# Kernel optimization log

Hardware: AMD Instinct MI355X
Metric: run time of the kernel (lower is better)

The kernel has to match this reference:

```python
import jax, jax.numpy as jnp
import numpy as np

BASE_P = 0.99
MIN_P = 0.9


def setup_inputs() -> dict:
    key = jax.random.key(0)
    k1, k2, k3 = jax.random.split(key, 3)
    B, T, C = 32, 4096, 256
    return {
        "student_latents": jax.random.normal(k1, (B, T, C), dtype=jnp.float32),
        "teacher_latents": jax.random.normal(k2, (B, T, C), dtype=jnp.float32),
        "risk_coef": jax.random.uniform(k3, (B,), dtype=jnp.float32),
    }


def reference(student_latents, teacher_latents, risk_coef):
    # 1) Epistemic uncertainty: per-token MSE between student and teacher  [B, T]
    delta = jnp.mean((student_latents - teacher_latents) ** 2, axis=-1)
    uncertainty = jnp.clip(delta * 2.0, 0.0, 1.0)
    # 2) Distrust = max(U, risk * U)  [B, T]
    distrust = jnp.maximum(uncertainty, risk_coef[:, None] * uncertainty)
    # 3) Dynamic percentile per sample  [B]
    distrust_b = jnp.mean(distrust, axis=1)
    p_eff = BASE_P - (BASE_P - MIN_P) * distrust_b
    # 4) Per-sample quantile threshold of |x| over flattened (T*C), then clamp.
    B = student_latents.shape[0]
    s = jnp.abs(student_latents).reshape(B, -1).astype(jnp.float32)
    # torch detaches before quantile -> no gradient through the threshold
    thresh = jax.lax.stop_gradient(
        jax.vmap(lambda a, q: jnp.quantile(a, q))(s, p_eff.astype(jnp.float32))
    )  # [B], linear interpolation matches torch.quantile default
    t = thresh[:, None, None].astype(student_latents.dtype)
    return jnp.clip(student_latents, -t, t)
```

## Files before the change

kernel.cpp:

```cpp
#include <hip/hip_runtime.h>
#include <stdint.h>

#define B_ 32
#define T_ 4096
#define C_ 256
#define N_ (T_*C_)
#define NB 8192

#define HIST_BYTES (B_*NB*4)
#define USUM_OFF   (HIST_BYTES)
#define THR_OFF    (USUM_OFF + 128)

__global__ __launch_bounds__(512, 6) void k1_uncert_hist(
    const float* __restrict__ s, const float* __restrict__ t,
    float* __restrict__ usum, unsigned* __restrict__ ghist)
{
    __shared__ unsigned lh[NB];
    __shared__ float wu[8];
    const int tid = threadIdx.x;
    #pragma unroll
    for (int k = tid; k < NB; k += 512) lh[k] = 0;
    __syncthreads();

    const int b = blockIdx.x >> 5;
    const size_t base4 = (size_t)blockIdx.x * 8192;
    const float4* s4 = (const float4*)s + base4;
    const float4* t4 = (const float4*)t + base4;
    const int lane = tid & 63, wid = tid >> 6;

    float uacc = 0.f;
    #pragma unroll 2
    for (int it = 0; it < 8; ++it) {
        const int i0 = it*1024 + wid*128 + lane;
        float4 a0 = s4[i0];
        float4 a1 = s4[i0 + 64];
        float4 c0 = t4[i0];
        float4 c1 = t4[i0 + 64];

        float d0 = a0.x-c0.x, d1 = a0.y-c0.y, d2 = a0.z-c0.z, d3 = a0.w-c0.w;
        float sum0 = d0*d0 + d1*d1 + d2*d2 + d3*d3;
        float e0 = a1.x-c1.x, e1 = a1.y-c1.y, e2 = a1.z-c1.z, e3 = a1.w-c1.w;
        float sum1 = e0*e0 + e1*e1 + e2*e2 + e3*e3;

        atomicAdd(&lh[(__float_as_uint(a0.x) & 0x7fffffffu) >> 18], 1u);
        atomicAdd(&lh[(__float_as_uint(a0.y) & 0x7fffffffu) >> 18], 1u);
        atomicAdd(&lh[(__float_as_uint(a0.z) & 0x7fffffffu) >> 18], 1u);
        atomicAdd(&lh[(__float_as_uint(a0.w) & 0x7fffffffu) >> 18], 1u);
        atomicAdd(&lh[(__float_as_uint(a1.x) & 0x7fffffffu) >> 18], 1u);
        atomicAdd(&lh[(__float_as_uint(a1.y) & 0x7fffffffu) >> 18], 1u);
        atomicAdd(&lh[(__float_as_uint(a1.z) & 0x7fffffffu) >> 18], 1u);
        atomicAdd(&lh[(__float_as_uint(a1.w) & 0x7fffffffu) >> 18], 1u);

        #pragma unroll
        for (int m = 1; m < 64; m <<= 1) {
            sum0 += __shfl_xor(sum0, m, 64);
            sum1 += __shfl_xor(sum1, m, 64);
        }
        if (lane == 0)
            uacc += fminf(sum0 * (1.0f/128.0f), 1.0f)
                  + fminf(sum1 * (1.0f/128.0f), 1.0f);
    }
    if (lane == 0) wu[wid] = uacc;
    __syncthreads();
    if (tid == 0) {
        float a = 0.f;
        #pragma unroll
        for (int w = 0; w < 8; ++w) a += wu[w];
        atomicAdd(&usum[b], a);
    }
    unsigned* gh = ghist + (size_t)b * NB;
    #pragma unroll
    for (int k = tid; k < NB; k += 512) {
        unsigned c = lh[k];
        if (c) atomicAdd(&gh[k], c);
    }
}

__global__ __launch_bounds__(256) void k2_thresh(
    const unsigned* __restrict__ ghist, const float* __restrict__ usum,
    const float* __restrict__ risk, float* __restrict__ thr)
{
    __shared__ unsigned lh[NB];
    __shared__ unsigned part[256];
    __shared__ unsigned pref[257];
    const int b = blockIdx.x, tid = threadIdx.x;
    const unsigned* gh = ghist + (size_t)b * NB;
    for (int j = tid; j < NB; j += 256) lh[j] = gh[j];
    __syncthreads();
    unsigned sl = 0;
    #pragma unroll
    for (int k = 0; k < 32; ++k) sl += lh[tid*32 + k];
    part[tid] = sl;
    __syncthreads();
    if (tid == 0) {
        unsigned acc = 0;
        for (int i = 0; i < 256; ++i) { pref[i] = acc; acc += part[i]; }
        pref[256] = acc;

        float distrust = usum[b] * fmaxf(1.f, risk[b]) * (1.0f/(float)T_);
        double p = 0.99 - 0.09 * (double)distrust;
        double pos = p * (double)(N_ - 1);
        unsigned i0 = (unsigned)pos;
        float g = (float)(pos - (double)i0);

        auto orderstat = [&](unsigned rk) -> float {
            int seg = 0;
            while (seg < 255 && pref[seg+1] <= rk) ++seg;
            unsigned cum = pref[seg];
            int bin = seg*32 + 31;
            unsigned cnt = 1;
            #pragma unroll
            for (int k = 0; k < 32; ++k) {
                unsigned c = lh[seg*32 + k];
                if (cum + c > rk) { bin = seg*32 + k; cnt = c; break; }
                cum += c;
            }
            float lo = __uint_as_float((unsigned)bin << 18);
            float hi = __uint_as_float((unsigned)(bin + 1) << 18);
            unsigned j = rk - cum;
            return lo + ((float)(j + 1) / (float)(cnt + 1)) * (hi - lo);
        };
        float v0 = orderstat(i0);
        float v1 = orderstat(i0 + 1);
        thr[b] = v0 + g * (v1 - v0);
    }
}

__global__ __launch_bounds__(256) void k3_clip(
    const float* __restrict__ s, const float* __restrict__ thr,
    float* __restrict__ out)
{
    const size_t idx4 = (size_t)blockIdx.x * 256 + threadIdx.x;
    const int b = (int)(idx4 >> 18);
    const float t = thr[b];
    float4 a = ((const float4*)s)[idx4];
    a.x = fminf(fmaxf(a.x, -t), t);
    a.y = fminf(fmaxf(a.y, -t), t);
    a.z = fminf(fmaxf(a.z, -t), t);
    a.w = fminf(fmaxf(a.w, -t), t);
    ((float4*)out)[idx4] = a;
}

extern "C" void kernel_launch(void* const* d_in, const int* in_sizes, int n_in,
                              void* d_out, int out_size, void* d_ws, size_t ws_size,
                              hipStream_t stream) {
    const float* s    = (const float*)d_in[0];
    const float* t    = (const float*)d_in[1];
    const float* risk = (const float*)d_in[2];
    float* out = (float*)d_out;
    char* ws = (char*)d_ws;

    unsigned* hist = (unsigned*)(ws);
    float*    usum = (float*)(ws + USUM_OFF);
    float*    thr  = (float*)(ws + THR_OFF);

    hipMemsetAsync(ws, 0, HIST_BYTES + 256, stream);

    k1_uncert_hist<<<B_*32, 512, 0, stream>>>(s, t, usum, hist);
    k2_thresh<<<B_, 256, 0, stream>>>(hist, usum, risk, thr);
    k3_clip<<<B_*N_/4/256, 256, 0, stream>>>(s, thr, out);
}
```

Baseline: 367.8 us.

## Pack histogram counters, prefetch loads, parallelize threshold scan, widen clip kernel

```diff
diff --git a/kernel.cpp b/kernel.cpp
--- a/kernel.cpp
+++ b/kernel.cpp
@@ -11,56 +11,82 @@
 #define USUM_OFF   (HIST_BYTES)
 #define THR_OFF    (USUM_OFF + 128)
 
-__global__ __launch_bounds__(512, 6) void k1_uncert_hist(
+typedef float f32x4 __attribute__((ext_vector_type(4)));
+
+__global__ __launch_bounds__(512, 8) void k1_uncert_hist(
     const float* __restrict__ s, const float* __restrict__ t,
     float* __restrict__ usum, unsigned* __restrict__ ghist)
 {
-    __shared__ unsigned lh[NB];
+    __shared__ unsigned lhist[4096];
+    __shared__ float part[64*65];
     __shared__ float wu[8];
     const int tid = threadIdx.x;
     #pragma unroll
-    for (int k = tid; k < NB; k += 512) lh[k] = 0;
-    __syncthreads();
-
-    const int b = blockIdx.x >> 5;
-    const size_t base4 = (size_t)blockIdx.x * 8192;
-    const float4* s4 = (const float4*)s + base4;
-    const float4* t4 = (const float4*)t + base4;
+    for (int k = tid; k < 4096; k += 512) lhist[k] = 0;
+    __syncthreads();
+
+    const int b = blockIdx.x >> 6;
+    const size_t base4 = (size_t)blockIdx.x * 4096;
+    const f32x4* s4 = (const f32x4*)s + base4;
+    const f32x4* t4 = (const f32x4*)t + base4;
     const int lane = tid & 63, wid = tid >> 6;
 
-    float uacc = 0.f;
-    #pragma unroll 2
-    for (int it = 0; it < 8; ++it) {
-        const int i0 = it*1024 + wid*128 + lane;
-        float4 a0 = s4[i0];
-        float4 a1 = s4[i0 + 64];
-        float4 c0 = t4[i0];
-        float4 c1 = t4[i0 + 64];
-
-        float d0 = a0.x-c0.x, d1 = a0.y-c0.y, d2 = a0.z-c0.z, d3 = a0.w-c0.w;
-        float sum0 = d0*d0 + d1*d1 + d2*d2 + d3*d3;
-        float e0 = a1.x-c1.x, e1 = a1.y-c1.y, e2 = a1.z-c1.z, e3 = a1.w-c1.w;
-        float sum1 = e0*e0 + e1*e1 + e2*e2 + e3*e3;
-
-        atomicAdd(&lh[(__float_as_uint(a0.x) & 0x7fffffffu) >> 18], 1u);
-        atomicAdd(&lh[(__float_as_uint(a0.y) & 0x7fffffffu) >> 18], 1u);
-        atomicAdd(&lh[(__float_as_uint(a0.z) & 0x7fffffffu) >> 18], 1u);
-        atomicAdd(&lh[(__float_as_uint(a0.w) & 0x7fffffffu) >> 18], 1u);
-        atomicAdd(&lh[(__float_as_uint(a1.x) & 0x7fffffffu) >> 18], 1u);
-        atomicAdd(&lh[(__float_as_uint(a1.y) & 0x7fffffffu) >> 18], 1u);
-        atomicAdd(&lh[(__float_as_uint(a1.z) & 0x7fffffffu) >> 18], 1u);
-        atomicAdd(&lh[(__float_as_uint(a1.w) & 0x7fffffffu) >> 18], 1u);
-
-        #pragma unroll
-        for (int m = 1; m < 64; m <<= 1) {
-            sum0 += __shfl_xor(sum0, m, 64);
-            sum1 += __shfl_xor(sum1, m, 64);
-        }
-        if (lane == 0)
-            uacc += fminf(sum0 * (1.0f/128.0f), 1.0f)
-                  + fminf(sum1 * (1.0f/128.0f), 1.0f);
-    }
-    if (lane == 0) wu[wid] = uacc;
+    int i = wid*128 + lane;
+    f32x4 a0 = s4[i];
+    f32x4 a1 = s4[i + 64];
+    f32x4 c0 = __builtin_nontemporal_load(t4 + i);
+    f32x4 c1 = __builtin_nontemporal_load(t4 + i + 64);
+
+    #pragma unroll
+    for (int it = 0; it < 4; ++it) {
+        f32x4 b0, b1, d0, d1;
+        const int inext = i + 1024;
+        if (it < 3) {
+            b0 = s4[inext];
+            b1 = s4[inext + 64];
+            d0 = __builtin_nontemporal_load(t4 + inext);
+            d1 = __builtin_nontemporal_load(t4 + inext + 64);
+        }
+
+        float dx = a0.x-c0.x, dy = a0.y-c0.y, dz = a0.z-c0.z, dw = a0.w-c0.w;
+        float sum0 = dx*dx + dy*dy + dz*dz + dw*dw;
+        float ex = a1.x-c1.x, ey = a1.y-c1.y, ez = a1.z-c1.z, ew = a1.w-c1.w;
+        float sum1 = ex*ex + ey*ey + ez*ez + ew*ew;
+
+        {
+            unsigned u;
+            u = __float_as_uint(a0.x); atomicAdd(&lhist[(u>>19)&0xFFF], 1u << (((u>>18)&1u)<<4));
+            u = __float_as_uint(a0.y); atomicAdd(&lhist[(u>>19)&0xFFF], 1u << (((u>>18)&1u)<<4));
+            u = __float_as_uint(a0.z); atomicAdd(&lhist[(u>>19)&0xFFF], 1u << (((u>>18)&1u)<<4));
+            u = __float_as_uint(a0.w); atomicAdd(&lhist[(u>>19)&0xFFF], 1u << (((u>>18)&1u)<<4));
+            u = __float_as_uint(a1.x); atomicAdd(&lhist[(u>>19)&0xFFF], 1u << (((u>>18)&1u)<<4));
+            u = __float_as_uint(a1.y); atomicAdd(&lhist[(u>>19)&0xFFF], 1u << (((u>>18)&1u)<<4));
+            u = __float_as_uint(a1.z); atomicAdd(&lhist[(u>>19)&0xFFF], 1u << (((u>>18)&1u)<<4));
+            u = __float_as_uint(a1.w); atomicAdd(&lhist[(u>>19)&0xFFF], 1u << (((u>>18)&1u)<<4));
+        }
+
+        const int tk = it*16 + wid*2;
+        part[tk*65 + lane]     = sum0;
+        part[(tk+1)*65 + lane] = sum1;
+
+        if (it < 3) { a0 = b0; a1 = b1; c0 = d0; c1 = d1; }
+        i = inext;
+    }
+    __syncthreads();
+
+    {
+        const int tok = tid >> 3, q = tid & 7;
+        const float* pp = &part[tok*65 + q*8];
+        float ps = pp[0]+pp[1]+pp[2]+pp[3]+pp[4]+pp[5]+pp[6]+pp[7];
+        ps += __shfl_xor(ps, 1, 64);
+        ps += __shfl_xor(ps, 2, 64);
+        ps += __shfl_xor(ps, 4, 64);
+        float u = fminf(ps * (1.0f/128.0f), 1.0f);
+        u += __shfl_xor(u, 8, 64);
+        u += __shfl_xor(u, 16, 64);
+        u += __shfl_xor(u, 32, 64);
+        if (lane == 0) wu[wid] = u;
+    }
     __syncthreads();
     if (tid == 0) {
         float a = 0.f;
@@ -68,11 +94,16 @@
         for (int w = 0; w < 8; ++w) a += wu[w];
         atomicAdd(&usum[b], a);
     }
+
     unsigned* gh = ghist + (size_t)b * NB;
     #pragma unroll
-    for (int k = tid; k < NB; k += 512) {
-        unsigned c = lh[k];
-        if (c) atomicAdd(&gh[k], c);
+    for (int w = tid; w < 4096; w += 512) {
+        const unsigned pc = lhist[w];
+        if (pc) {
+            const unsigned lo = pc & 0xFFFFu, hi = pc >> 16;
+            if (lo) atomicAdd(&gh[2*w],   lo);
+            if (hi) atomicAdd(&gh[2*w+1], hi);
+        }
     }
 }
 
@@ -81,64 +112,79 @@
     const float* __restrict__ risk, float* __restrict__ thr)
 {
     __shared__ unsigned lh[NB];
-    __shared__ unsigned part[256];
-    __shared__ unsigned pref[257];
+    __shared__ unsigned sc[256];
+    __shared__ float res[2];
     const int b = blockIdx.x, tid = threadIdx.x;
     const unsigned* gh = ghist + (size_t)b * NB;
     for (int j = tid; j < NB; j += 256) lh[j] = gh[j];
     __syncthreads();
-    unsigned sl = 0;
-    #pragma unroll
-    for (int k = 0; k < 32; ++k) sl += lh[tid*32 + k];
-    part[tid] = sl;
-    __syncthreads();
-    if (tid == 0) {
-        unsigned acc = 0;
-        for (int i = 0; i < 256; ++i) { pref[i] = acc; acc += part[i]; }
-        pref[256] = acc;
-
-        float distrust = usum[b] * fmaxf(1.f, risk[b]) * (1.0f/(float)T_);
-        double p = 0.99 - 0.09 * (double)distrust;
-        double pos = p * (double)(N_ - 1);
-        unsigned i0 = (unsigned)pos;
-        float g = (float)(pos - (double)i0);
-
-        auto orderstat = [&](unsigned rk) -> float {
-            int seg = 0;
-            while (seg < 255 && pref[seg+1] <= rk) ++seg;
-            unsigned cum = pref[seg];
-            int bin = seg*32 + 31;
-            unsigned cnt = 1;
+
+    unsigned p = 0;
+    #pragma unroll
+    for (int k = 0; k < 32; ++k) p += lh[tid*32 + k];
+    sc[tid] = p;
+    __syncthreads();
+    #pragma unroll
+    for (int d = 1; d < 256; d <<= 1) {
+        unsigned v = (tid >= d) ? sc[tid - d] : 0u;
+        __syncthreads();
+        sc[tid] += v;
+        __syncthreads();
+    }
+    const unsigned incl = sc[tid];
+    const unsigned excl = incl - p;
+
+    const float distrust = usum[b] * fmaxf(1.f, risk[b]) * (1.0f/(float)T_);
+    const double pq  = 0.99 - 0.09 * (double)distrust;
+    const double pos = pq * (double)(N_ - 1);
+    const unsigned i0 = (unsigned)pos;
+    const float g = (float)(pos - (double)i0);
+
+    #pragma unroll
+    for (int r = 0; r < 2; ++r) {
+        const unsigned rk = i0 + (unsigned)r;
+        if (excl <= rk && rk < incl) {
+            unsigned cum = excl, cnt = 1;
+            int bin = tid*32 + 31;
             #pragma unroll
             for (int k = 0; k < 32; ++k) {
-                unsigned c = lh[seg*32 + k];
-                if (cum + c > rk) { bin = seg*32 + k; cnt = c; break; }
+                const unsigned c = lh[tid*32 + k];
+                if (cum + c > rk) { bin = tid*32 + k; cnt = c; break; }
                 cum += c;
             }
-            float lo = __uint_as_float((unsigned)bin << 18);
-            float hi = __uint_as_float((unsigned)(bin + 1) << 18);
-            unsigned j = rk - cum;
-            return lo + ((float)(j + 1) / (float)(cnt + 1)) * (hi - lo);
-        };
-        float v0 = orderstat(i0);
-        float v1 = orderstat(i0 + 1);
-        thr[b] = v0 + g * (v1 - v0);
-    }
+            const float lo = __uint_as_float((unsigned)bin << 18);
+            const float hi = __uint_as_float((unsigned)(bin + 1) << 18);
+            const unsigned j = rk - cum;
+            res[r] = lo + ((float)(j + 1) / (float)(cnt + 1)) * (hi - lo);
+        }
+    }
+    __syncthreads();
+    if (tid == 0) thr[b] = res[0] + g * (res[1] - res[0]);
 }
 
 __global__ __launch_bounds__(256) void k3_clip(
     const float* __restrict__ s, const float* __restrict__ thr,
     float* __restrict__ out)
 {
-    const size_t idx4 = (size_t)blockIdx.x * 256 + threadIdx.x;
-    const int b = (int)(idx4 >> 18);
+    const int bid = blockIdx.x;
+    const int b = bid >> 7;
     const float t = thr[b];
-    float4 a = ((const float4*)s)[idx4];
-    a.x = fminf(fmaxf(a.x, -t), t);
-    a.y = fminf(fmaxf(a.y, -t), t);
-    a.z = fminf(fmaxf(a.z, -t), t);
-    a.w = fminf(fmaxf(a.w, -t), t);
-    ((float4*)out)[idx4] = a;
+    const size_t base = (size_t)bid * 2048 + threadIdx.x;
+    const f32x4* s4 = (const f32x4*)s;
+    f32x4* o4 = (f32x4*)out;
+
+    f32x4 v[8];
+    #pragma unroll
+    for (int k = 0; k < 8; ++k) v[k] = s4[base + (size_t)k*256];
+    #pragma unroll
+    for (int k = 0; k < 8; ++k) {
+        f32x4 a = v[k];
+        a.x = fminf(fmaxf(a.x, -t), t);
+        a.y = fminf(fmaxf(a.y, -t), t);
+        a.z = fminf(fmaxf(a.z, -t), t);
+        a.w = fminf(fmaxf(a.w, -t), t);
+        __builtin_nontemporal_store(a, o4 + base + (size_t)k*256);
+    }
 }
 
 extern "C" void kernel_launch(void* const* d_in, const int* in_sizes, int n_in,
@@ -156,7 +202,7 @@
 
     hipMemsetAsync(ws, 0, HIST_BYTES + 256, stream);
 
-    k1_uncert_hist<<<B_*32, 512, 0, stream>>>(s, t, usum, hist);
+    k1_uncert_hist<<<2048, 512, 0, stream>>>(s, t, usum, hist);
     k2_thresh<<<B_, 256, 0, stream>>>(hist, usum, risk, thr);
-    k3_clip<<<B_*N_/4/256, 256, 0, stream>>>(s, thr, out);
-}
+    k3_clip<<<4096, 256, 0, stream>>>(s, thr, out);
+}
```

After: 338.3 us. -8.0%, faster.
